# Kernel optimization log

Measured on AMD Instinct MI355X. Metric: run time of the kernel, lower is better.

The kernel has to match this reference:

```python
import jax, jax.numpy as jnp
import numpy as np

H = 256      # hidden_size
B = 32       # batch
T = 4096     # timesteps / graph nodes
E = 8192     # edges per graph
PATH = 1
EXPAND_WEIGHT = 0.1
MODE = 'son'


def setup_inputs() -> dict:
    key = jax.random.key(0)
    ks = jax.random.split(key, 6)
    hidden = jax.random.normal(ks[0], (B, H), jnp.float32)
    encoder_outputs = jax.random.normal(ks[1], (T, B, H), jnp.float32)
    edges_src = jax.random.randint(ks[2], (B, E), 0, T)
    edges_dst = jax.random.randint(ks[3], (B, E), 0, T)
    # nn.Linear(2H, 2H) params (kaiming-uniform-ish scale) and the v vector
    lim = 1.0 / np.sqrt(2 * H)
    W_attn = jax.random.uniform(ks[4], (2 * H, 2 * H), jnp.float32, -lim, lim)
    b_attn = jnp.zeros((2 * H,), jnp.float32)
    v = jax.random.uniform(ks[5], (2 * H,), jnp.float32, -lim, lim)
    return {"hidden": hidden, "encoder_outputs": encoder_outputs,
            "edges_src": edges_src, "edges_dst": edges_dst,
            "W_attn": W_attn, "b_attn": b_attn, "v": v}


def reference(hidden, encoder_outputs, edges_src, edges_dst, W_attn, b_attn, v):
    Bb, Hh = hidden.shape
    Tt = encoder_outputs.shape[0]
    # h: [B, T, H] (hidden repeated over timesteps); enc: [B, T, H]
    h = jnp.broadcast_to(hidden[:, None, :], (Bb, Tt, Hh))
    enc = jnp.transpose(encoder_outputs, (1, 0, 2))
    # score: tanh(Linear(cat)) then v . energy -> [B, T]
    energy = jnp.tanh(jnp.concatenate([h, enc], axis=2) @ W_attn.T + b_attn)
    scores = jnp.einsum('btd,d->bt', energy, v)
    w = jax.nn.softmax(scores, axis=1)
    # expand_attn: scatter-add along graph edges, skipping consecutive (y == x+1)
    mask = (edges_dst != edges_src + 1).astype(w.dtype)  # [B, E]
    def scatter(wb, src, dst, m):
        if MODE == 'son':
            return jnp.zeros_like(wb).at[dst].add(wb[src] * m)
        else:
            return jnp.zeros_like(wb).at[src].add(wb[dst] * m)
    for _ in range(PATH):
        w = jax.vmap(scatter)(w, edges_src, edges_dst, mask) * EXPAND_WEIGHT
    return w[:, None, :]  # [B, 1, T]
```

## Files before the change

### kernel.cpp

```cpp
#include <hip/hip_runtime.h>
#include <hip/hip_bf16.h>

typedef __attribute__((ext_vector_type(8))) short bf16x8;
typedef __attribute__((ext_vector_type(4))) float f32x4;

#define HD 256
#define NB 32
#define NT 4096
#define NE 8192
#define N2 512

static __device__ __forceinline__ unsigned short f2bf(float f) {
  unsigned int u = __float_as_uint(f);
  u += 0x7fff + ((u >> 16) & 1);
  return (unsigned short)(u >> 16);
}
static __device__ __forceinline__ short4 cvt4(float4 a) {
  return make_short4((short)f2bf(a.x), (short)f2bf(a.y),
                     (short)f2bf(a.z), (short)f2bf(a.w));
}
static __device__ __forceinline__ float fast_tanh(float x) {
  float e = __builtin_amdgcn_exp2f(x * 2.8853900817779268f);
  return __builtin_fmaf(-2.f, __builtin_amdgcn_rcpf(e + 1.f), 1.f);
}
static __device__ __forceinline__ bf16x8 pack8(float4 a, float4 b) {
  union { bf16x8 v; unsigned int u[4]; } r;
  r.u[0] = (__float_as_uint(a.y) & 0xffff0000u) | (__float_as_uint(a.x) >> 16);
  r.u[1] = (__float_as_uint(a.w) & 0xffff0000u) | (__float_as_uint(a.z) >> 16);
  r.u[2] = (__float_as_uint(b.y) & 0xffff0000u) | (__float_as_uint(b.x) >> 16);
  r.u[3] = (__float_as_uint(b.w) & 0xffff0000u) | (__float_as_uint(b.z) >> 16);
  return r.v;
}

__global__ __launch_bounds__(256) void prep(
    const float* __restrict__ hidden, const float* __restrict__ Wattn,
    const float* __restrict__ battn, float* __restrict__ cvecT,
    short* __restrict__ WbfT) {
  const int tid = threadIdx.x;
  if (blockIdx.x < 256) {
    __shared__ float Ws[64 * 260];
    __shared__ float Hs[HD];
    const int chunk = blockIdx.x & 7;
    const int b = blockIdx.x >> 3;
#pragma unroll
    for (int it = 0; it < 16; ++it) {
      int f = it * 1024 + tid * 4;
      int i = f >> 8, k = f & 255;
      float4 w4 = *(const float4*)(Wattn + (chunk * 64 + i) * N2 + k);
      *(float4*)&Ws[i * 260 + k] = w4;
    }
    if (tid < 64)
      *(float4*)&Hs[tid * 4] = *(const float4*)(hidden + b * HD + tid * 4);
    __syncthreads();
    const int nl = tid >> 2;
    const int kb = (tid & 3) * 64;
    float sum = 0.f;
#pragma unroll
    for (int z = 0; z < 64; z += 4) {
      float4 h4 = *(const float4*)&Hs[kb + z];
      float4 w4 = *(const float4*)&Ws[nl * 260 + kb + z];
      sum = fmaf(h4.x, w4.x, sum);
      sum = fmaf(h4.y, w4.y, sum);
      sum = fmaf(h4.z, w4.z, sum);
      sum = fmaf(h4.w, w4.w, sum);
    }
    sum += __shfl_xor(sum, 1, 64);
    sum += __shfl_xor(sum, 2, 64);
    if ((tid & 3) == 0)
      cvecT[(chunk * 64 + nl) * NB + b] = sum + battn[chunk * 64 + nl];
  } else {
    int f = (blockIdx.x - 256) * 1024 + tid * 4;
    int n = f >> 8, k = f & 255;
    float4 w4 = *(const float4*)(Wattn + n * N2 + HD + k);
    *(short4*)(WbfT + ((k >> 5) * 512 + n) * 32 + (k & 31)) = cvt4(w4);
  }
}

static __device__ __forceinline__ void bload(bf16x8* dst, const short* __restrict__ Wp,
                                             int nbase, int q, int kk) {
  const short* base = Wp + (kk * 512 + nbase) * 32 + q * 8;
#pragma unroll
  for (int nf = 0; nf < 4; ++nf)
    dst[nf] = *(const bf16x8*)(base + nf * 16 * 32);
}

static __device__ __forceinline__ void kstep(f32x4 acc[4][4], const short* Abf,
                                             const bf16x8* b, int rb, int m, int q,
                                             int ks) {
#pragma unroll
  for (int mi = 0; mi < 4; ++mi) {
    const int r = rb + mi * 16 + m;
    const int cc = ks * 4 + q;
    const int slot = (cc & ~7) | ((cc & 7) ^ (r & 7));
    bf16x8 af = *(const bf16x8*)&Abf[r * 256 + slot * 8];
#pragma unroll
    for (int nf = 0; nf < 4; ++nf)
      acc[mi][nf] =
          __builtin_amdgcn_mfma_f32_16x16x32_bf16(af, b[nf], acc[mi][nf], 0, 0, 0);
  }
}

__global__ __launch_bounds__(1024, 4) void score_gemm(
    const float* __restrict__ enc, const short* __restrict__ WbfT,
    const float* __restrict__ cvecT, const float* __restrict__ vvec,
    float* __restrict__ scores) {
  __shared__ short Abf[128 * 256];
  __shared__ float part[16][64];
  const int tid = threadIdx.x;
  const int w = tid >> 6, lane = tid & 63, q = lane >> 4, m = lane & 15;
  const int g = w >> 3, wl = w & 7;
  const int row0 = blockIdx.x * 128;

#pragma unroll
  for (int i = 0; i < 4; ++i) {
    const int gg = i * 1024 + tid;
    const int r = gg >> 5, c = gg & 31;
    const float* src = enc + (row0 + r) * HD + c * 8;
    float4 a0 = *(const float4*)src;
    float4 a1 = *(const float4*)(src + 4);
    const int slot = (c & ~7) | ((c & 7) ^ (r & 7));
    *(bf16x8*)&Abf[r * 256 + slot * 8] = pack8(a0, a1);
  }

  f32x4 acc[4][4];
#pragma unroll
  for (int mi = 0; mi < 4; ++mi)
#pragma unroll
    for (int nf = 0; nf < 4; ++nf) acc[mi][nf] = (f32x4){0.f, 0.f, 0.f, 0.f};

  const int nbase = wl * 64 + m;
  const int rb = g * 64;
  bf16x8 b0[4], b1[4];
  bload(b0, WbfT, nbase, q, 0);

  __syncthreads();

#pragma unroll 1
  for (int ks2 = 0; ks2 < 4; ++ks2) {
    const int ks = ks2 * 2;
    bload(b1, WbfT, nbase, q, ks + 1);
    kstep(acc, Abf, b0, rb, m, q, ks);
    if (ks2 < 3) bload(b0, WbfT, nbase, q, ks + 2);
    kstep(acc, Abf, b1, rb, m, q, ks + 1);
  }

  float p[4][4];
#pragma unroll
  for (int mi = 0; mi < 4; ++mi)
#pragma unroll
    for (int j = 0; j < 4; ++j) p[mi][j] = 0.f;

#pragma unroll
  for (int nf = 0; nf < 4; ++nf) {
    const int n = wl * 64 + nf * 16 + m;
    const float vv = vvec[n];
    const f32x4 cvA = *(const f32x4*)(cvecT + n * NB + 4 * q);
    const f32x4 cvB = *(const f32x4*)(cvecT + n * NB + 16 + 4 * q);
#pragma unroll
    for (int mi = 0; mi < 4; ++mi) {
      const f32x4 cv = (mi & 1) ? cvB : cvA;
#pragma unroll
      for (int j = 0; j < 4; ++j)
        p[mi][j] += fast_tanh(acc[mi][nf][j] + cv[j]) * vv;
    }
  }
#pragma unroll
  for (int mi = 0; mi < 4; ++mi) {
#pragma unroll
    for (int j = 0; j < 4; ++j) {
      float e = p[mi][j];
      e += __shfl_xor(e, 1, 64);
      e += __shfl_xor(e, 2, 64);
      e += __shfl_xor(e, 4, 64);
      e += __shfl_xor(e, 8, 64);
      if (m == 0) part[w][mi * 16 + 4 * q + j] = e;
    }
  }
  __syncthreads();
  if (tid < 128) {
    const int r = row0 + tid;
    float s = 0.f;
#pragma unroll
    for (int ww = 0; ww < 8; ++ww) s += part[(tid >> 6) * 8 + ww][tid & 63];
    scores[(r & 31) * NT + (r >> 5)] = s;
  }
}

__global__ __launch_bounds__(1024) void softmax_scatter(
    const float* __restrict__ sc, const int* __restrict__ esrc,
    const int* __restrict__ edst, float* __restrict__ out) {
  __shared__ float wls[NT];
  __shared__ float accs[NT];
  __shared__ float rtmp[16];
  __shared__ float rmax, rinv;
  const int b = blockIdx.x;
  const int tid = threadIdx.x;
  const int wid = tid >> 6, lane = tid & 63;

  float s[4];
  float mx = -1e30f;
#pragma unroll
  for (int p = 0; p < 4; ++p) {
    s[p] = sc[b * NT + tid + p * 1024];
    mx = fmaxf(mx, s[p]);
  }
#pragma unroll
  for (int d = 32; d >= 1; d >>= 1) mx = fmaxf(mx, __shfl_xor(mx, d, 64));
  if (lane == 0) rtmp[wid] = mx;
  __syncthreads();
  if (tid == 0) {
    float mm = rtmp[0];
#pragma unroll
    for (int i = 1; i < 16; ++i) mm = fmaxf(mm, rtmp[i]);
    rmax = mm;
  }
  __syncthreads();
  mx = rmax;
  float e[4];
  float sm = 0.f;
#pragma unroll
  for (int p = 0; p < 4; ++p) {
    e[p] = __expf(s[p] - mx);
    sm += e[p];
  }
#pragma unroll
  for (int d = 32; d >= 1; d >>= 1) sm += __shfl_xor(sm, d, 64);
  if (lane == 0) rtmp[wid] = sm;
  __syncthreads();
  if (tid == 0) {
    float tt = 0.f;
#pragma unroll
    for (int i = 0; i < 16; ++i) tt += rtmp[i];
    rinv = 0.1f / tt;
  }
  __syncthreads();
  const float inv = rinv;
#pragma unroll
  for (int p = 0; p < 4; ++p) {
    wls[tid + p * 1024] = e[p] * inv;
    accs[tid + p * 1024] = 0.f;
  }
  __syncthreads();
#pragma unroll
  for (int i = 0; i < 8; ++i) {
    const int eid = b * NE + tid + i * 1024;
    const int ss = esrc[eid];
    const int dd = edst[eid];
    const float wv = wls[ss];
    if (dd != ss + 1) atomicAdd(&accs[dd], wv);
  }
  __syncthreads();
#pragma unroll
  for (int p = 0; p < 4; ++p)
    out[b * NT + tid + p * 1024] = accs[tid + p * 1024];
}

extern "C" void kernel_launch(void* const* d_in, const int* in_sizes, int n_in,
                              void* d_out, int out_size, void* d_ws, size_t ws_size,
                              hipStream_t stream) {
  const float* hidden = (const float*)d_in[0];
  const float* enc    = (const float*)d_in[1];
  const int*   esrc   = (const int*)d_in[2];
  const int*   edst   = (const int*)d_in[3];
  const float* Wattn  = (const float*)d_in[4];
  const float* battn  = (const float*)d_in[5];
  const float* vvec   = (const float*)d_in[6];
  float* out = (float*)d_out;

  char* ws = (char*)d_ws;
  float* cvecT  = (float*)ws;
  short* WbfT   = (short*)(ws + 65536);
  float* scores = (float*)(ws + 65536 + 262144);

  prep<<<384, 256, 0, stream>>>(hidden, Wattn, battn, cvecT, WbfT);
  score_gemm<<<(NB * NT) / 128, 1024, 0, stream>>>(enc, WbfT, cvecT, vvec, scores);
  softmax_scatter<<<NB, 1024, 0, stream>>>(scores, esrc, edst, out);
}
```

Measured before the change: 274.5 us.

## Double-buffer encoder tiles via direct global-to-LDS loads in persistent score GEMM

The score GEMM becomes a persistent kernel: 512 blocks of 512 threads, each looping over four 64-row tiles. The next fp32 encoder tile is loaded straight into LDS with global_load_lds while the current tile is computed, and the bf16 conversion moves to the point where MFMA operands are read. This is meant to hide global load latency behind compute and skip the register round-trip of the staging copy. In exchange it uses fp32 LDS (double the footprint), repacks A on every k-step, reloads the W operands for every tile, and adds extra barriers per tile.

```diff
diff --git a/kernel.cpp b/kernel.cpp
--- a/kernel.cpp
+++ b/kernel.cpp
@@ -31,6 +31,11 @@
   r.u[3] = (__float_as_uint(b.w) & 0xffff0000u) | (__float_as_uint(b.z) >> 16);
   return r.v;
 }
+
+#define GLDS16(g, l)                                                       \
+  __builtin_amdgcn_global_load_lds(                                        \
+      (const __attribute__((address_space(1))) unsigned int*)(g),          \
+      (__attribute__((address_space(3))) unsigned int*)(l), 16, 0, 0)
 
 __global__ __launch_bounds__(256) void prep(
     const float* __restrict__ hidden, const float* __restrict__ Wattn,
@@ -84,15 +89,15 @@
     dst[nf] = *(const bf16x8*)(base + nf * 16 * 32);
 }
 
-static __device__ __forceinline__ void kstep(f32x4 acc[4][4], const short* Abf,
-                                             const bf16x8* b, int rb, int m, int q,
-                                             int ks) {
+static __device__ __forceinline__ void kstep(f32x4 acc[4][4], const float4* As4p,
+                                             const bf16x8* b, int m, int q, int ks) {
 #pragma unroll
   for (int mi = 0; mi < 4; ++mi) {
-    const int r = rb + mi * 16 + m;
-    const int cc = ks * 4 + q;
-    const int slot = (cc & ~7) | ((cc & 7) ^ (r & 7));
-    bf16x8 af = *(const bf16x8*)&Abf[r * 256 + slot * 8];
+    const int r = mi * 16 + m;
+    const int cb = r * 64 + ks * 8;
+    float4 a0 = As4p[cb + ((2 * q) ^ (r & 7))];
+    float4 a1 = As4p[cb + ((2 * q + 1) ^ (r & 7))];
+    bf16x8 af = pack8(a0, a1);
 #pragma unroll
     for (int nf = 0; nf < 4; ++nf)
       acc[mi][nf] =
@@ -100,89 +105,99 @@
   }
 }
 
-__global__ __launch_bounds__(1024, 4) void score_gemm(
+__global__ __launch_bounds__(512, 2) void score_gemm(
     const float* __restrict__ enc, const short* __restrict__ WbfT,
     const float* __restrict__ cvecT, const float* __restrict__ vvec,
     float* __restrict__ scores) {
-  __shared__ short Abf[128 * 256];
-  __shared__ float part[16][64];
+  __shared__ float4 As4[2 * 64 * 64];
+  __shared__ float part[8][64];
   const int tid = threadIdx.x;
   const int w = tid >> 6, lane = tid & 63, q = lane >> 4, m = lane & 15;
-  const int g = w >> 3, wl = w & 7;
-  const int row0 = blockIdx.x * 128;
-
-#pragma unroll
-  for (int i = 0; i < 4; ++i) {
-    const int gg = i * 1024 + tid;
-    const int r = gg >> 5, c = gg & 31;
-    const float* src = enc + (row0 + r) * HD + c * 8;
-    float4 a0 = *(const float4*)src;
-    float4 a1 = *(const float4*)(src + 4);
-    const int slot = (c & ~7) | ((c & 7) ^ (r & 7));
-    *(bf16x8*)&Abf[r * 256 + slot * 8] = pack8(a0, a1);
-  }
-
-  f32x4 acc[4][4];
-#pragma unroll
-  for (int mi = 0; mi < 4; ++mi)
-#pragma unroll
-    for (int nf = 0; nf < 4; ++nf) acc[mi][nf] = (f32x4){0.f, 0.f, 0.f, 0.f};
-
-  const int nbase = wl * 64 + m;
-  const int rb = g * 64;
-  bf16x8 b0[4], b1[4];
-  bload(b0, WbfT, nbase, q, 0);
-
+  const int nbase = w * 64 + m;
+  const int base_row = blockIdx.x * 256;
+
+#pragma unroll
+  for (int i = 0; i < 8; ++i) {
+    const int r = i * 8 + w;
+    const int gc = (lane & ~7) | ((lane & 7) ^ (r & 7));
+    GLDS16(enc + (base_row + r) * HD + gc * 4, &As4[r * 64]);
+  }
   __syncthreads();
 
 #pragma unroll 1
-  for (int ks2 = 0; ks2 < 4; ++ks2) {
-    const int ks = ks2 * 2;
-    bload(b1, WbfT, nbase, q, ks + 1);
-    kstep(acc, Abf, b0, rb, m, q, ks);
-    if (ks2 < 3) bload(b0, WbfT, nbase, q, ks + 2);
-    kstep(acc, Abf, b1, rb, m, q, ks + 1);
-  }
-
-  float p[4][4];
-#pragma unroll
-  for (int mi = 0; mi < 4; ++mi)
-#pragma unroll
-    for (int j = 0; j < 4; ++j) p[mi][j] = 0.f;
-
-#pragma unroll
-  for (int nf = 0; nf < 4; ++nf) {
-    const int n = wl * 64 + nf * 16 + m;
-    const float vv = vvec[n];
-    const f32x4 cvA = *(const f32x4*)(cvecT + n * NB + 4 * q);
-    const f32x4 cvB = *(const f32x4*)(cvecT + n * NB + 16 + 4 * q);
+  for (int tt = 0; tt < 4; ++tt) {
+    const int p = tt & 1;
+    const int row0 = base_row + tt * 64;
+    const float4* As4p = As4 + p * 4096;
+
+    if (tt < 3) {
+#pragma unroll
+      for (int i = 0; i < 8; ++i) {
+        const int r = i * 8 + w;
+        const int gc = (lane & ~7) | ((lane & 7) ^ (r & 7));
+        GLDS16(enc + (row0 + 64 + r) * HD + gc * 4,
+               &As4[(1 - p) * 4096 + r * 64]);
+      }
+    }
+
+    f32x4 acc[4][4];
+#pragma unroll
+    for (int mi = 0; mi < 4; ++mi)
+#pragma unroll
+      for (int nf = 0; nf < 4; ++nf) acc[mi][nf] = (f32x4){0.f, 0.f, 0.f, 0.f};
+
+    bf16x8 b0[4], b1[4];
+    bload(b0, WbfT, nbase, q, 0);
+#pragma unroll
+    for (int ks2 = 0; ks2 < 4; ++ks2) {
+      const int ks = ks2 * 2;
+      bload(b1, WbfT, nbase, q, ks + 1);
+      kstep(acc, As4p, b0, m, q, ks);
+      if (ks2 < 3) bload(b0, WbfT, nbase, q, ks + 2);
+      kstep(acc, As4p, b1, m, q, ks + 1);
+    }
+
+    float pr[4][4];
+#pragma unroll
+    for (int mi = 0; mi < 4; ++mi)
+#pragma unroll
+      for (int j = 0; j < 4; ++j) pr[mi][j] = 0.f;
+
+#pragma unroll
+    for (int nf = 0; nf < 4; ++nf) {
+      const int n = w * 64 + nf * 16 + m;
+      const float vv = vvec[n];
+      const f32x4 cvA = *(const f32x4*)(cvecT + n * NB + 4 * q);
+      const f32x4 cvB = *(const f32x4*)(cvecT + n * NB + 16 + 4 * q);
+#pragma unroll
+      for (int mi = 0; mi < 4; ++mi) {
+        const f32x4 cv = (mi & 1) ? cvB : cvA;
+#pragma unroll
+        for (int j = 0; j < 4; ++j)
+          pr[mi][j] += fast_tanh(acc[mi][nf][j] + cv[j]) * vv;
+      }
+    }
 #pragma unroll
     for (int mi = 0; mi < 4; ++mi) {
-      const f32x4 cv = (mi & 1) ? cvB : cvA;
-#pragma unroll
-      for (int j = 0; j < 4; ++j)
-        p[mi][j] += fast_tanh(acc[mi][nf][j] + cv[j]) * vv;
-    }
-  }
-#pragma unroll
-  for (int mi = 0; mi < 4; ++mi) {
-#pragma unroll
-    for (int j = 0; j < 4; ++j) {
-      float e = p[mi][j];
-      e += __shfl_xor(e, 1, 64);
-      e += __shfl_xor(e, 2, 64);
-      e += __shfl_xor(e, 4, 64);
-      e += __shfl_xor(e, 8, 64);
-      if (m == 0) part[w][mi * 16 + 4 * q + j] = e;
-    }
-  }
-  __syncthreads();
-  if (tid < 128) {
-    const int r = row0 + tid;
-    float s = 0.f;
-#pragma unroll
-    for (int ww = 0; ww < 8; ++ww) s += part[(tid >> 6) * 8 + ww][tid & 63];
-    scores[(r & 31) * NT + (r >> 5)] = s;
+#pragma unroll
+      for (int j = 0; j < 4; ++j) {
+        float e = pr[mi][j];
+        e += __shfl_xor(e, 1, 64);
+        e += __shfl_xor(e, 2, 64);
+        e += __shfl_xor(e, 4, 64);
+        e += __shfl_xor(e, 8, 64);
+        if (m == 0) part[w][mi * 16 + 4 * q + j] = e;
+      }
+    }
+    __syncthreads();
+    if (tid < 64) {
+      const int r = row0 + tid;
+      float s = 0.f;
+#pragma unroll
+      for (int ww = 0; ww < 8; ++ww) s += part[ww][tid];
+      scores[(r & 31) * NT + (r >> 5)] = s;
+    }
+    __syncthreads();
   }
 }
 
@@ -273,6 +288,6 @@
   float* scores = (float*)(ws + 65536 + 262144);
 
   prep<<<384, 256, 0, stream>>>(hidden, Wattn, battn, cvecT, WbfT);
-  score_gemm<<<(NB * NT) / 128, 1024, 0, stream>>>(enc, WbfT, cvecT, vvec, scores);
+  score_gemm<<<512, 512, 0, stream>>>(enc, WbfT, cvecT, vvec, scores);
   softmax_scatter<<<NB, 1024, 0, stream>>>(scores, esrc, edst, out);
 }
```

Measured after the change: 292.0 us. +6.4%, slower.
